# Optimization experiments

Hardware: AMD Instinct MI355X
Metric: run time of the kernel (lower is better)

The kernel has to match this reference:

```python
import jax, jax.numpy as jnp
import numpy as np

B, IN, H, A, K = 8192, 2048, 256, 8192, 512

def setup_inputs() -> dict:
    key = jax.random.key(0)
    ks = jax.random.split(key, 8)
    s1, s2, s3 = 1.0/np.sqrt(IN), 1.0/np.sqrt(H), 1.0/np.sqrt(H)
    return {
        "x": jax.random.normal(ks[0], (B, IN), dtype=jnp.float32),
        "possible_moves": jax.random.randint(ks[1], (B, K), 0, A, dtype=jnp.int64),
        "W1": jax.random.uniform(ks[2], (IN, H), jnp.float32, -s1, s1),
        "b1": jax.random.uniform(ks[3], (H,), jnp.float32, -s1, s1),
        "W2": jax.random.uniform(ks[4], (H, H), jnp.float32, -s2, s2),
        "b2": jax.random.uniform(ks[5], (H,), jnp.float32, -s2, s2),
        "W3": jax.random.uniform(ks[6], (H, A), jnp.float32, -s3, s3),
        "b3": jax.random.uniform(ks[7], (A,), jnp.float32, -s3, s3),
    }

def reference(x, possible_moves, W1, b1, W2, b2, W3, b3):
    h = jax.nn.relu(x @ W1 + b1)
    h = jax.nn.relu(h @ W2 + b2)
    q = h @ W3 + b3                      # [B, A]
    # build per-sample legal-move mask via scatter (replaces torch python loop)
    rows = jnp.arange(q.shape[0])[:, None]
    mask = jnp.zeros(q.shape, q.dtype).at[rows, possible_moves].set(1.0)
    filtered = q * mask
    # faithful to torch: any exact-zero entry (illegal OR q==0) becomes -inf
    return jnp.where(filtered == 0, -jnp.inf, filtered)
```

## Files before the change

kernel.cpp:

```cpp
#include <hip/hip_runtime.h>
#include <math.h>
#include <stdint.h>

#define B_DIM   8192
#define IN_DIM  2048
#define H_DIM   256
#define A_DIM   8192
#define K_MOVES 512

#define NEG_SENTINEL (-3.0e38f)

typedef __attribute__((ext_vector_type(8))) short          short8;
typedef __attribute__((ext_vector_type(8))) unsigned short ushort8;
typedef __attribute__((ext_vector_type(4))) unsigned short ushort4v;
typedef __attribute__((ext_vector_type(4))) float          f32x4;

#define MFMA_16x16x32_BF16(a, b, c) \
    __builtin_amdgcn_mfma_f32_16x16x32_bf16((a), (b), (c), 0, 0, 0)

__device__ __forceinline__ unsigned short f2bf(float f) {
    union { float f; unsigned int u; } v; v.f = f;
    unsigned int r = v.u + 0x7fffu + ((v.u >> 16) & 1u);
    return (unsigned short)(r >> 16);
}

__global__ void zero_u64_kernel(unsigned long long* __restrict__ p, int n) {
    int i = blockIdx.x * 256 + threadIdx.x;
    if (i < n) p[i] = 0ULL;
}

__global__ void scatter_mask_kernel(const int* __restrict__ pm,
                                    unsigned long long* __restrict__ mask) {
    int i = blockIdx.x * 256 + threadIdx.x;
    int row = i / K_MOVES;
    int mv  = pm[i];
    if (mv < 0) mv = 0;
    if (mv >= A_DIM) mv = A_DIM - 1;
    atomicOr(&mask[(size_t)row * (A_DIM / 64) + (mv >> 6)],
             1ULL << (mv & 63));
}

__global__ void cvt_bf16_kernel(const float* __restrict__ in,
                                unsigned short* __restrict__ out, int n8) {
    int i = blockIdx.x * 256 + threadIdx.x;
    if (i >= n8) return;
    const float4* p = (const float4*)in + (size_t)i * 2;
    float4 a = p[0], b = p[1];
    ushort8 o;
    o[0] = f2bf(a.x); o[1] = f2bf(a.y); o[2] = f2bf(a.z); o[3] = f2bf(a.w);
    o[4] = f2bf(b.x); o[5] = f2bf(b.y); o[6] = f2bf(b.z); o[7] = f2bf(b.w);
    *(ushort8*)(out + (size_t)i * 8) = o;
}

__global__ __launch_bounds__(256)
void transpose_cvt_kernel(const float* __restrict__ in,
                          unsigned short* __restrict__ out, int R, int C) {
    __shared__ unsigned short tile[32][33];
    int x = blockIdx.x * 32 + threadIdx.x;
#pragma unroll
    for (int i = 0; i < 32; i += 8) {
        int y = blockIdx.y * 32 + threadIdx.y + i;
        tile[threadIdx.y + i][threadIdx.x] = f2bf(in[(size_t)y * C + x]);
    }
    __syncthreads();
    int ox = blockIdx.y * 32 + threadIdx.x;
#pragma unroll
    for (int i = 0; i < 32; i += 8) {
        int oy = blockIdx.x * 32 + threadIdx.y + i;
        out[(size_t)oy * R + ox] = tile[threadIdx.x][threadIdx.y + i];
    }
}

template <int BM, int RELU, int MASKED, typename OutT>
__global__ __launch_bounds__(256)
void gemm_bt_mfma(const unsigned short* __restrict__ A,
                  const unsigned short* __restrict__ Bt,
                  const float* __restrict__ bias,
                  OutT* __restrict__ C,
                  const unsigned long long* __restrict__ mask,
                  int M, int N, int K) {
    constexpr int MI = BM / 32;
    __shared__ __align__(16) unsigned short As[BM * 32];
    __shared__ __align__(16) unsigned short Bs[128 * 32];

    const int tid  = threadIdx.x;
    const int wave = tid >> 6;
    const int lane = tid & 63;
    const int quad = lane >> 4;
    const int tl   = lane & 15;
    const int wm   = wave >> 1;
    const int wn   = wave & 1;
    const int row0 = blockIdx.y * BM;
    const int col0 = blockIdx.x * 128;

    f32x4 acc[MI][4];
#pragma unroll
    for (int i = 0; i < MI; ++i)
#pragma unroll
        for (int j = 0; j < 4; ++j) acc[i][j] = {0.f, 0.f, 0.f, 0.f};

    for (int k0 = 0; k0 < K; k0 += 32) {
#pragma unroll
        for (int p = 0; p < BM / 64; ++p) {
            const int c = p * 256 + tid;
            const unsigned short* g =
                A + (size_t)(row0 + (c >> 2)) * K + k0 + (c & 3) * 8;
            __builtin_amdgcn_global_load_lds(
                (const __attribute__((address_space(1))) void*)g,
                (__attribute__((address_space(3))) void*)&As[(p * 256 + wave * 64) * 8],
                16, 0, 0);
        }
#pragma unroll
        for (int p = 0; p < 2; ++p) {
            const int c = p * 256 + tid;
            const unsigned short* g =
                Bt + (size_t)(col0 + (c >> 2)) * K + k0 + (c & 3) * 8;
            __builtin_amdgcn_global_load_lds(
                (const __attribute__((address_space(1))) void*)g,
                (__attribute__((address_space(3))) void*)&Bs[(p * 256 + wave * 64) * 8],
                16, 0, 0);
        }
        __syncthreads();

        short8 af[MI], bf[4];
#pragma unroll
        for (int i = 0; i < MI; ++i)
            af[i] = *(const short8*)&As[(wm * (BM / 2) + i * 16 + tl) * 32 + quad * 8];
#pragma unroll
        for (int j = 0; j < 4; ++j)
            bf[j] = *(const short8*)&Bs[(wn * 64 + j * 16 + tl) * 32 + quad * 8];

#pragma unroll
        for (int i = 0; i < MI; ++i)
#pragma unroll
            for (int j = 0; j < 4; ++j)
                acc[i][j] = MFMA_16x16x32_BF16(bf[j], af[i], acc[i][j]);
        __syncthreads();
    }

    float4 bj4[4];
#pragma unroll
    for (int j = 0; j < 4; ++j)
        bj4[j] = *(const float4*)&bias[col0 + wn * 64 + j * 16 + quad * 4];

#pragma unroll
    for (int i = 0; i < MI; ++i) {
        const int r = row0 + wm * (BM / 2) + i * 16 + tl;
        unsigned long long w = 0;
        if (MASKED) {
            w = mask[(size_t)r * (N >> 6) + (col0 >> 6) + wn];
        }
#pragma unroll
        for (int j = 0; j < 4; ++j) {
            float q[4];
#pragma unroll
            for (int reg = 0; reg < 4; ++reg) {
                float t = acc[i][j][reg] + ((const float*)&bj4[j])[reg];
                if (RELU) t = fmaxf(t, 0.f);
                if (MASKED) {
                    const int bit = j * 16 + quad * 4 + reg;
                    bool legal = (w >> bit) & 1ULL;
                    bool ok = legal && (t != 0.f) && (fabsf(t) < 1.0e30f);
                    t = ok ? t : NEG_SENTINEL;
                }
                q[reg] = t;
            }
            const size_t off = (size_t)r * N + col0 + wn * 64 + j * 16 + quad * 4;
            if constexpr (sizeof(OutT) == 2) {
                ushort4v o;
                o[0] = f2bf(q[0]); o[1] = f2bf(q[1]);
                o[2] = f2bf(q[2]); o[3] = f2bf(q[3]);
                *(ushort4v*)&C[off] = o;
            } else {
                float4 o = make_float4(q[0], q[1], q[2], q[3]);
                *(float4*)&C[off] = o;
            }
        }
    }
}

extern "C" void kernel_launch(void* const* d_in, const int* in_sizes, int n_in,
                              void* d_out, int out_size, void* d_ws, size_t ws_size,
                              hipStream_t stream) {
    const float* x  = (const float*)d_in[0];
    const int*   pm = (const int*)d_in[1];
    const float* W1 = (const float*)d_in[2];
    const float* b1 = (const float*)d_in[3];
    const float* W2 = (const float*)d_in[4];
    const float* b2 = (const float*)d_in[5];
    const float* W3 = (const float*)d_in[6];
    const float* b3 = (const float*)d_in[7];
    float* out = (float*)d_out;

    char* ws = (char*)d_ws;
    unsigned long long* mask = (unsigned long long*)ws;
    unsigned short* xb  = (unsigned short*)(ws + (8ull  << 20));
    unsigned short* W1t = (unsigned short*)(ws + (40ull << 20));
    unsigned short* W2t = (unsigned short*)(ws + (41ull << 20));
    unsigned short* W3t = (unsigned short*)(ws + (42ull << 20));
    unsigned short* h1b = (unsigned short*)(ws + (46ull << 20));
    unsigned short* h2b = (unsigned short*)(ws + (50ull << 20));

    zero_u64_kernel<<<(B_DIM * (A_DIM / 64)) / 256, 256, 0, stream>>>(
        mask, B_DIM * (A_DIM / 64));
    scatter_mask_kernel<<<(B_DIM * K_MOVES) / 256, 256, 0, stream>>>(pm, mask);

    cvt_bf16_kernel<<<(B_DIM * IN_DIM / 8) / 256, 256, 0, stream>>>(
        x, xb, B_DIM * IN_DIM / 8);
    transpose_cvt_kernel<<<dim3(H_DIM / 32, IN_DIM / 32), dim3(32, 8), 0, stream>>>(
        W1, W1t, IN_DIM, H_DIM);
    transpose_cvt_kernel<<<dim3(H_DIM / 32, H_DIM / 32), dim3(32, 8), 0, stream>>>(
        W2, W2t, H_DIM, H_DIM);
    transpose_cvt_kernel<<<dim3(A_DIM / 32, H_DIM / 32), dim3(32, 8), 0, stream>>>(
        W3, W3t, H_DIM, A_DIM);

    gemm_bt_mfma<64, 1, 0, unsigned short>
        <<<dim3(H_DIM / 128, B_DIM / 64), 256, 0, stream>>>(
        xb, W1t, b1, h1b, nullptr, B_DIM, H_DIM, IN_DIM);

    gemm_bt_mfma<64, 1, 0, unsigned short>
        <<<dim3(H_DIM / 128, B_DIM / 64), 256, 0, stream>>>(
        h1b, W2t, b2, h2b, nullptr, B_DIM, H_DIM, H_DIM);

    gemm_bt_mfma<128, 0, 1, float>
        <<<dim3(A_DIM / 128, B_DIM / 128), 256, 0, stream>>>(
        h2b, W3t, b3, out, mask, B_DIM, A_DIM, H_DIM);
}
```

Baseline: 517.0 us.

## Fuse x conversion into GEMM1, build mask in LDS, merge transposes

Result: faster. 432.7 us (-16.3%).

```diff
diff --git a/kernel.cpp b/kernel.cpp
--- a/kernel.cpp
+++ b/kernel.cpp
@@ -24,114 +24,220 @@
     return (unsigned short)(r >> 16);
 }
 
-__global__ void zero_u64_kernel(unsigned long long* __restrict__ p, int n) {
-    int i = blockIdx.x * 256 + threadIdx.x;
-    if (i < n) p[i] = 0ULL;
-}
-
-__global__ void scatter_mask_kernel(const int* __restrict__ pm,
-                                    unsigned long long* __restrict__ mask) {
-    int i = blockIdx.x * 256 + threadIdx.x;
-    int row = i / K_MOVES;
-    int mv  = pm[i];
-    if (mv < 0) mv = 0;
-    if (mv >= A_DIM) mv = A_DIM - 1;
-    atomicOr(&mask[(size_t)row * (A_DIM / 64) + (mv >> 6)],
-             1ULL << (mv & 63));
-}
-
-__global__ void cvt_bf16_kernel(const float* __restrict__ in,
-                                unsigned short* __restrict__ out, int n8) {
-    int i = blockIdx.x * 256 + threadIdx.x;
-    if (i >= n8) return;
-    const float4* p = (const float4*)in + (size_t)i * 2;
-    float4 a = p[0], b = p[1];
+__device__ __forceinline__ ushort8 pack8(float4 a, float4 b) {
     ushort8 o;
     o[0] = f2bf(a.x); o[1] = f2bf(a.y); o[2] = f2bf(a.z); o[3] = f2bf(a.w);
     o[4] = f2bf(b.x); o[5] = f2bf(b.y); o[6] = f2bf(b.z); o[7] = f2bf(b.w);
-    *(ushort8*)(out + (size_t)i * 8) = o;
+    return o;
 }
 
 __global__ __launch_bounds__(256)
-void transpose_cvt_kernel(const float* __restrict__ in,
-                          unsigned short* __restrict__ out, int R, int C) {
+void scatter_mask_kernel(const int* __restrict__ pm,
+                         unsigned long long* __restrict__ mask) {
+    __shared__ unsigned long long lm[A_DIM / 64];
+    const int row = blockIdx.x;
+    const int tid = threadIdx.x;
+    if (tid < 128) lm[tid] = 0ULL;
+    __syncthreads();
+    const int* p = pm + (size_t)row * K_MOVES;
+#pragma unroll
+    for (int s = 0; s < K_MOVES / 256; ++s) {
+        int mv = p[s * 256 + tid];
+        if (mv < 0) mv = 0;
+        if (mv >= A_DIM) mv = A_DIM - 1;
+        atomicOr(&lm[mv >> 6], 1ULL << (mv & 63));
+    }
+    __syncthreads();
+    if (tid < 128) mask[(size_t)row * 128 + tid] = lm[tid];
+}
+
+__global__ __launch_bounds__(256)
+void transpose3_kernel(const float* __restrict__ W1, unsigned short* __restrict__ W1t,
+                       const float* __restrict__ W2, unsigned short* __restrict__ W2t,
+                       const float* __restrict__ W3, unsigned short* __restrict__ W3t) {
     __shared__ unsigned short tile[32][33];
-    int x = blockIdx.x * 32 + threadIdx.x;
+    const int bid = blockIdx.x;
+    const float* in; unsigned short* out; int R, C, bx, by;
+    if (bid < 512)      { in = W1; out = W1t; R = IN_DIM; C = H_DIM;
+                          bx = bid % 8;          by = bid / 8; }
+    else if (bid < 576) { in = W2; out = W2t; R = H_DIM;  C = H_DIM;
+                          int t = bid - 512; bx = t % 8;   by = t / 8; }
+    else                { in = W3; out = W3t; R = H_DIM;  C = A_DIM;
+                          int t = bid - 576; bx = t % 256; by = t / 256; }
+    const int tx = threadIdx.x, ty = threadIdx.y;
+    int x = bx * 32 + tx;
 #pragma unroll
     for (int i = 0; i < 32; i += 8) {
-        int y = blockIdx.y * 32 + threadIdx.y + i;
-        tile[threadIdx.y + i][threadIdx.x] = f2bf(in[(size_t)y * C + x]);
+        int y = by * 32 + ty + i;
+        tile[ty + i][tx] = f2bf(in[(size_t)y * C + x]);
     }
     __syncthreads();
-    int ox = blockIdx.y * 32 + threadIdx.x;
+    int ox = by * 32 + tx;
 #pragma unroll
     for (int i = 0; i < 32; i += 8) {
-        int oy = blockIdx.x * 32 + threadIdx.y + i;
-        out[(size_t)oy * R + ox] = tile[threadIdx.x][threadIdx.y + i];
-    }
-}
-
-template <int BM, int RELU, int MASKED, typename OutT>
+        int oy = bx * 32 + ty + i;
+        out[(size_t)oy * R + ox] = tile[tx][ty + i];
+    }
+}
+
+template <typename AT>
 __global__ __launch_bounds__(256)
-void gemm_bt_mfma(const unsigned short* __restrict__ A,
-                  const unsigned short* __restrict__ Bt,
-                  const float* __restrict__ bias,
-                  OutT* __restrict__ C,
-                  const unsigned long long* __restrict__ mask,
-                  int M, int N, int K) {
-    constexpr int MI = BM / 32;
-    __shared__ __align__(16) unsigned short As[BM * 32];
+void gemm_small(const AT* __restrict__ A,
+                const unsigned short* __restrict__ Bt,
+                const float* __restrict__ bias,
+                unsigned short* __restrict__ C,
+                int M, int N, int K) {
+    constexpr bool A_F32 = (sizeof(AT) == 4);
+    constexpr int LDA = 72;
+    __shared__ __align__(16) unsigned short As[64 * LDA];
+    __shared__ __align__(16) unsigned short Bs[64 * LDA];
+
+    const int tid  = threadIdx.x;
+    const int wave = tid >> 6, lane = tid & 63;
+    const int quad = lane >> 4, tl = lane & 15;
+    const int wm = wave >> 1,  wn = wave & 1;
+    const int row0 = blockIdx.y * 64, col0 = blockIdx.x * 64;
+    const int sr = tid >> 2;
+    const int sk = (tid & 3) * 16;
+
+    f32x4 acc[2][2];
+#pragma unroll
+    for (int i = 0; i < 2; ++i)
+#pragma unroll
+        for (int j = 0; j < 2; ++j) acc[i][j] = {0.f, 0.f, 0.f, 0.f};
+
+    const AT* Ap             = A  + (size_t)(row0 + sr) * K + sk;
+    const unsigned short* Bp = Bt + (size_t)(col0 + sr) * K + sk;
+
+    float4  pa[4];
+    ushort8 pa8[2];
+    ushort8 pb[2];
+
+    if constexpr (A_F32) {
+#pragma unroll
+        for (int q = 0; q < 4; ++q) pa[q] = ((const float4*)Ap)[q];
+    } else {
+        pa8[0] = ((const ushort8*)Ap)[0];
+        pa8[1] = ((const ushort8*)Ap)[1];
+    }
+    pb[0] = ((const ushort8*)Bp)[0];
+    pb[1] = ((const ushort8*)Bp)[1];
+
+    const int iters = K >> 6;
+    for (int t = 0; t < iters; ++t) {
+        if constexpr (A_F32) {
+            *(ushort8*)&As[sr * LDA + sk]     = pack8(pa[0], pa[1]);
+            *(ushort8*)&As[sr * LDA + sk + 8] = pack8(pa[2], pa[3]);
+        } else {
+            *(ushort8*)&As[sr * LDA + sk]     = pa8[0];
+            *(ushort8*)&As[sr * LDA + sk + 8] = pa8[1];
+        }
+        *(ushort8*)&Bs[sr * LDA + sk]     = pb[0];
+        *(ushort8*)&Bs[sr * LDA + sk + 8] = pb[1];
+        __syncthreads();
+
+        if (t + 1 < iters) {
+            const AT* ap             = Ap + (t + 1) * 64;
+            const unsigned short* bp = Bp + (t + 1) * 64;
+            if constexpr (A_F32) {
+#pragma unroll
+                for (int q = 0; q < 4; ++q) pa[q] = ((const float4*)ap)[q];
+            } else {
+                pa8[0] = ((const ushort8*)ap)[0];
+                pa8[1] = ((const ushort8*)ap)[1];
+            }
+            pb[0] = ((const ushort8*)bp)[0];
+            pb[1] = ((const ushort8*)bp)[1];
+        }
+
+#pragma unroll
+        for (int ks = 0; ks < 2; ++ks) {
+            short8 af[2], bf[2];
+#pragma unroll
+            for (int i = 0; i < 2; ++i)
+                af[i] = *(const short8*)&As[(wm * 32 + i * 16 + tl) * LDA + ks * 32 + quad * 8];
+#pragma unroll
+            for (int j = 0; j < 2; ++j)
+                bf[j] = *(const short8*)&Bs[(wn * 32 + j * 16 + tl) * LDA + ks * 32 + quad * 8];
+#pragma unroll
+            for (int i = 0; i < 2; ++i)
+#pragma unroll
+                for (int j = 0; j < 2; ++j)
+                    acc[i][j] = MFMA_16x16x32_BF16(bf[j], af[i], acc[i][j]);
+        }
+        __syncthreads();
+    }
+
+    float4 bj4[2];
+#pragma unroll
+    for (int j = 0; j < 2; ++j)
+        bj4[j] = *(const float4*)&bias[col0 + wn * 32 + j * 16 + quad * 4];
+#pragma unroll
+    for (int i = 0; i < 2; ++i) {
+        const int r = row0 + wm * 32 + i * 16 + tl;
+#pragma unroll
+        for (int j = 0; j < 2; ++j) {
+            ushort4v o;
+#pragma unroll
+            for (int reg = 0; reg < 4; ++reg) {
+                float q = acc[i][j][reg] + ((const float*)&bj4[j])[reg];
+                o[reg] = f2bf(fmaxf(q, 0.f));
+            }
+            *(ushort4v*)&C[(size_t)r * N + col0 + wn * 32 + j * 16 + quad * 4] = o;
+        }
+    }
+}
+
+__global__ __launch_bounds__(256)
+void gemm_masked(const unsigned short* __restrict__ A,
+                 const unsigned short* __restrict__ Bt,
+                 const float* __restrict__ bias,
+                 float* __restrict__ C,
+                 const unsigned long long* __restrict__ mask,
+                 int M, int N, int K) {
+    __shared__ __align__(16) unsigned short As[128 * 32];
     __shared__ __align__(16) unsigned short Bs[128 * 32];
 
     const int tid  = threadIdx.x;
-    const int wave = tid >> 6;
-    const int lane = tid & 63;
-    const int quad = lane >> 4;
-    const int tl   = lane & 15;
-    const int wm   = wave >> 1;
-    const int wn   = wave & 1;
-    const int row0 = blockIdx.y * BM;
-    const int col0 = blockIdx.x * 128;
-
-    f32x4 acc[MI][4];
-#pragma unroll
-    for (int i = 0; i < MI; ++i)
+    const int wave = tid >> 6, lane = tid & 63;
+    const int quad = lane >> 4, tl = lane & 15;
+    const int wm = wave >> 1,  wn = wave & 1;
+    const int row0 = blockIdx.y * 128, col0 = blockIdx.x * 128;
+
+    f32x4 acc[4][4];
+#pragma unroll
+    for (int i = 0; i < 4; ++i)
 #pragma unroll
         for (int j = 0; j < 4; ++j) acc[i][j] = {0.f, 0.f, 0.f, 0.f};
 
     for (int k0 = 0; k0 < K; k0 += 32) {
 #pragma unroll
-        for (int p = 0; p < BM / 64; ++p) {
+        for (int p = 0; p < 2; ++p) {
             const int c = p * 256 + tid;
-            const unsigned short* g =
+            const unsigned short* ga =
                 A + (size_t)(row0 + (c >> 2)) * K + k0 + (c & 3) * 8;
             __builtin_amdgcn_global_load_lds(
-                (const __attribute__((address_space(1))) void*)g,
+                (const __attribute__((address_space(1))) void*)ga,
                 (__attribute__((address_space(3))) void*)&As[(p * 256 + wave * 64) * 8],
                 16, 0, 0);
-        }
-#pragma unroll
-        for (int p = 0; p < 2; ++p) {
-            const int c = p * 256 + tid;
-            const unsigned short* g =
+            const unsigned short* gb =
                 Bt + (size_t)(col0 + (c >> 2)) * K + k0 + (c & 3) * 8;
             __builtin_amdgcn_global_load_lds(
-                (const __attribute__((address_space(1))) void*)g,
+                (const __attribute__((address_space(1))) void*)gb,
                 (__attribute__((address_space(3))) void*)&Bs[(p * 256 + wave * 64) * 8],
                 16, 0, 0);
         }
         __syncthreads();
 
-        short8 af[MI], bf[4];
-#pragma unroll
-        for (int i = 0; i < MI; ++i)
-            af[i] = *(const short8*)&As[(wm * (BM / 2) + i * 16 + tl) * 32 + quad * 8];
+        short8 af[4], bf[4];
+#pragma unroll
+        for (int i = 0; i < 4; ++i)
+            af[i] = *(const short8*)&As[(wm * 64 + i * 16 + tl) * 32 + quad * 8];
 #pragma unroll
         for (int j = 0; j < 4; ++j)
             bf[j] = *(const short8*)&Bs[(wn * 64 + j * 16 + tl) * 32 + quad * 8];
-
-#pragma unroll
-        for (int i = 0; i < MI; ++i)
+#pragma unroll
+        for (int i = 0; i < 4; ++i)
 #pragma unroll
             for (int j = 0; j < 4; ++j)
                 acc[i][j] = MFMA_16x16x32_BF16(bf[j], af[i], acc[i][j]);
@@ -144,37 +250,22 @@
         bj4[j] = *(const float4*)&bias[col0 + wn * 64 + j * 16 + quad * 4];
 
 #pragma unroll
-    for (int i = 0; i < MI; ++i) {
-        const int r = row0 + wm * (BM / 2) + i * 16 + tl;
-        unsigned long long w = 0;
-        if (MASKED) {
-            w = mask[(size_t)r * (N >> 6) + (col0 >> 6) + wn];
-        }
+    for (int i = 0; i < 4; ++i) {
+        const int r = row0 + wm * 64 + i * 16 + tl;
+        const unsigned long long w = mask[(size_t)r * (N >> 6) + (col0 >> 6) + wn];
 #pragma unroll
         for (int j = 0; j < 4; ++j) {
             float q[4];
 #pragma unroll
             for (int reg = 0; reg < 4; ++reg) {
-                float t = acc[i][j][reg] + ((const float*)&bj4[j])[reg];
-                if (RELU) t = fmaxf(t, 0.f);
-                if (MASKED) {
-                    const int bit = j * 16 + quad * 4 + reg;
-                    bool legal = (w >> bit) & 1ULL;
-                    bool ok = legal && (t != 0.f) && (fabsf(t) < 1.0e30f);
-                    t = ok ? t : NEG_SENTINEL;
-                }
-                q[reg] = t;
+                float v = acc[i][j][reg] + ((const float*)&bj4[j])[reg];
+                const int bit = j * 16 + quad * 4 + reg;
+                bool legal = (w >> bit) & 1ULL;
+                bool ok = legal && (v != 0.f) && (fabsf(v) < 1.0e30f);
+                q[reg] = ok ? v : NEG_SENTINEL;
             }
-            const size_t off = (size_t)r * N + col0 + wn * 64 + j * 16 + quad * 4;
-            if constexpr (sizeof(OutT) == 2) {
-                ushort4v o;
-                o[0] = f2bf(q[0]); o[1] = f2bf(q[1]);
-                o[2] = f2bf(q[2]); o[3] = f2bf(q[3]);
-                *(ushort4v*)&C[off] = o;
-            } else {
-                float4 o = make_float4(q[0], q[1], q[2], q[3]);
-                *(float4*)&C[off] = o;
-            }
+            *(float4*)&C[(size_t)r * N + col0 + wn * 64 + j * 16 + quad * 4] =
+                make_float4(q[0], q[1], q[2], q[3]);
         }
     }
 }
@@ -194,35 +285,22 @@
 
     char* ws = (char*)d_ws;
     unsigned long long* mask = (unsigned long long*)ws;
-    unsigned short* xb  = (unsigned short*)(ws + (8ull  << 20));
-    unsigned short* W1t = (unsigned short*)(ws + (40ull << 20));
-    unsigned short* W2t = (unsigned short*)(ws + (41ull << 20));
-    unsigned short* W3t = (unsigned short*)(ws + (42ull << 20));
-    unsigned short* h1b = (unsigned short*)(ws + (46ull << 20));
-    unsigned short* h2b = (unsigned short*)(ws + (50ull << 20));
-
-    zero_u64_kernel<<<(B_DIM * (A_DIM / 64)) / 256, 256, 0, stream>>>(
-        mask, B_DIM * (A_DIM / 64));
-    scatter_mask_kernel<<<(B_DIM * K_MOVES) / 256, 256, 0, stream>>>(pm, mask);
-
-    cvt_bf16_kernel<<<(B_DIM * IN_DIM / 8) / 256, 256, 0, stream>>>(
-        x, xb, B_DIM * IN_DIM / 8);
-    transpose_cvt_kernel<<<dim3(H_DIM / 32, IN_DIM / 32), dim3(32, 8), 0, stream>>>(
-        W1, W1t, IN_DIM, H_DIM);
-    transpose_cvt_kernel<<<dim3(H_DIM / 32, H_DIM / 32), dim3(32, 8), 0, stream>>>(
-        W2, W2t, H_DIM, H_DIM);
-    transpose_cvt_kernel<<<dim3(A_DIM / 32, H_DIM / 32), dim3(32, 8), 0, stream>>>(
-        W3, W3t, H_DIM, A_DIM);
-
-    gemm_bt_mfma<64, 1, 0, unsigned short>
-        <<<dim3(H_DIM / 128, B_DIM / 64), 256, 0, stream>>>(
-        xb, W1t, b1, h1b, nullptr, B_DIM, H_DIM, IN_DIM);
-
-    gemm_bt_mfma<64, 1, 0, unsigned short>
-        <<<dim3(H_DIM / 128, B_DIM / 64), 256, 0, stream>>>(
-        h1b, W2t, b2, h2b, nullptr, B_DIM, H_DIM, H_DIM);
-
-    gemm_bt_mfma<128, 0, 1, float>
-        <<<dim3(A_DIM / 128, B_DIM / 128), 256, 0, stream>>>(
+    unsigned short* W1t = (unsigned short*)(ws + (8ull  << 20));
+    unsigned short* W2t = (unsigned short*)(ws + (9ull  << 20));
+    unsigned short* W3t = (unsigned short*)(ws + (10ull << 20));
+    unsigned short* h1b = (unsigned short*)(ws + (16ull << 20));
+    unsigned short* h2b = (unsigned short*)(ws + (20ull << 20));
+
+    transpose3_kernel<<<2624, dim3(32, 8), 0, stream>>>(W1, W1t, W2, W2t, W3, W3t);
+
+    scatter_mask_kernel<<<B_DIM, 256, 0, stream>>>(pm, mask);
+
+    gemm_small<float><<<dim3(H_DIM / 64, B_DIM / 64), 256, 0, stream>>>(
+        x, W1t, b1, h1b, B_DIM, H_DIM, IN_DIM);
+
+    gemm_small<unsigned short><<<dim3(H_DIM / 64, B_DIM / 64), 256, 0, stream>>>(
+        h1b, W2t, b2, h2b, B_DIM, H_DIM, H_DIM);
+
+    gemm_masked<<<dim3(A_DIM / 128, B_DIM / 128), 256, 0, stream>>>(
         h2b, W3t, b3, out, mask, B_DIM, A_DIM, H_DIM);
 }
```
